# Kernel optimization log

Hardware: AMD Instinct MI355X
Metric: run time of the kernel (lower is better)

## Reference

```python
import jax, jax.numpy as jnp
import numpy as np

D_K = 64  # hardcoded in source module

def setup_inputs() -> dict:
    key = jax.random.key(0)
    kq, kk, kv, km = jax.random.split(key, 4)
    B, H, S, D = 2, 16, 2048, D_K
    Q = jax.random.normal(kq, (B, H, S, D), dtype=jnp.float32)
    K = jax.random.normal(kk, (B, H, S, D), dtype=jnp.float32)
    V = jax.random.normal(kv, (B, H, S, D), dtype=jnp.float32)
    # boolean mask: True positions are masked out (filled with -1e9)
    attn_mask = jax.random.randint(km, (B, H, S, S), 0, 2) == 1
    return {"Q": Q, "K": K, "V": V, "attn_mask": attn_mask}

def reference(Q, K, V, attn_mask):
    scale = 1.0 / np.sqrt(D_K).astype(np.float32)
    # scores: [B, H, S, S]
    scores = jnp.einsum('bhqd,bhkd->bhqk', Q, K) * scale
    scores = jnp.where(attn_mask, jnp.float32(-1e9), scores)
    attn = jax.nn.softmax(scores, axis=-1)
    context = jnp.einsum('bhqk,bhkd->bhqd', attn, V)
    return context
```

## Files before the change

kernel.cpp:

```cpp
#include <hip/hip_runtime.h>

#define SEQ    2048
#define DK     64
#define QBLK   128
#define KVBLK  64
#define NTILE  (SEQ / KVBLK)
#define PITCH  72
#define PPITCH 72

typedef __attribute__((ext_vector_type(8))) __bf16 bf16x8;
typedef __attribute__((ext_vector_type(4))) __bf16 bf16x4;
typedef __attribute__((ext_vector_type(2))) __bf16 bf16x2;
typedef __attribute__((ext_vector_type(4))) float  f32x4;
typedef __attribute__((ext_vector_type(4))) int    i32x4;

template<int CTRL>
__device__ __forceinline__ float dpp_ror(float v) {
  int i = __builtin_bit_cast(int, v);
  int r = __builtin_amdgcn_update_dpp(i, i, CTRL, 0xf, 0xf, false);
  return __builtin_bit_cast(float, r);
}
__device__ __forceinline__ float grp16_max(float v) {
  v = fmaxf(v, dpp_ror<0x128>(v));
  v = fmaxf(v, dpp_ror<0x124>(v));
  v = fmaxf(v, dpp_ror<0x122>(v));
  v = fmaxf(v, dpp_ror<0x121>(v));
  return v;
}
__device__ __forceinline__ float grp16_sum(float v) {
  v += dpp_ror<0x128>(v);
  v += dpp_ror<0x124>(v);
  v += dpp_ror<0x122>(v);
  v += dpp_ror<0x121>(v);
  return v;
}

__device__ __forceinline__ void block_sync_lds() {
  asm volatile("s_waitcnt lgkmcnt(0)" ::: "memory");
  __builtin_amdgcn_sched_barrier(0);
  __builtin_amdgcn_s_barrier();
  __builtin_amdgcn_sched_barrier(0);
}

__global__ __launch_bounds__(256, 2)
void sdpa_fwd(const float* __restrict__ Q, const float* __restrict__ K,
              const float* __restrict__ V, const int* __restrict__ M,
              float* __restrict__ O)
{
  __shared__ __bf16 Klds[KVBLK][PITCH];
  __shared__ __bf16 Vt[DK][PITCH];
  __shared__ __bf16 Plds[4][32][PPITCH];

  const int tid  = threadIdx.x;
  const int w    = tid >> 6;
  const int lane = tid & 63;
  const int g    = lane >> 4;
  const int li   = lane & 15;

  const int bid = blockIdx.x;
  const int blk = (bid & 7) * 64 + (bid >> 3);
  const int qb  = blk & (SEQ / QBLK - 1);
  const int bh  = blk >> 4;

  const float* Qp = Q + (size_t)bh * SEQ * DK;
  const float* Kp = K + (size_t)bh * SEQ * DK;
  const float* Vp = V + (size_t)bh * SEQ * DK;
  const int*   Mp = M + (size_t)bh * SEQ * SEQ;
  float*       Op = O + (size_t)bh * SEQ * DK;

  const int q0 = qb * QBLK + w * 16;

  const int sk = tid >> 2;
  const int sd = (tid & 3) * 16;
  const int sj = ((sk & 3) << 4) | (sk >> 2);
  const int vk = (tid & 31) * 2;
  const int vd = (tid >> 5) * 8;

  bf16x8 qfrag[2][2];
  #pragma unroll
  for (int m = 0; m < 2; ++m) {
    const float qs = 0.125f * 1.44269504088896340736f;
    const float* qr = Qp + (size_t)(q0 + m * 64 + li) * DK + g * 8;
    #pragma unroll
    for (int h2 = 0; h2 < 2; ++h2) {
      f32x4 a = *(const f32x4*)(qr + h2 * 32);
      f32x4 b = *(const f32x4*)(qr + h2 * 32 + 4);
      bf16x8 f;
      #pragma unroll
      for (int e = 0; e < 4; ++e) { f[e] = (__bf16)(a[e] * qs); f[4 + e] = (__bf16)(b[e] * qs); }
      qfrag[m][h2] = f;
    }
  }

  f32x4 acc[2][4];
  #pragma unroll
  for (int m = 0; m < 2; ++m)
    #pragma unroll
    for (int c = 0; c < 4; ++c) acc[m][c] = (f32x4){0.f, 0.f, 0.f, 0.f};
  float m_r[2][4], l_r[2][4];
  #pragma unroll
  for (int m = 0; m < 2; ++m)
    #pragma unroll
    for (int r = 0; r < 4; ++r) { m_r[m][r] = -__builtin_inff(); l_r[m][r] = 0.f; }

  f32x4 kA[4], vA[4];
  i32x4 mA[8];

  {
    const float* ks  = Kp + (size_t)sk * DK + sd;
    const float* vs0 = Vp + (size_t)vk * DK + vd;
    const float* vs1 = Vp + (size_t)(vk + 1) * DK + vd;
    #pragma unroll
    for (int i = 0; i < 4; ++i) kA[i] = *(const f32x4*)(ks + 4 * i);
    vA[0] = *(const f32x4*)vs0; vA[1] = *(const f32x4*)(vs0 + 4);
    vA[2] = *(const f32x4*)vs1; vA[3] = *(const f32x4*)(vs1 + 4);
    #pragma unroll
    for (int m = 0; m < 2; ++m)
      #pragma unroll
      for (int r = 0; r < 4; ++r)
        mA[m * 4 + r] = __builtin_nontemporal_load(
            (const i32x4*)(Mp + (size_t)(q0 + m * 64 + 4 * g + r) * SEQ + li * 4));
  }

  for (int kt = 0; kt < NTILE; ++kt) {
    block_sync_lds();

    {
      bf16x8 klo, khi;
      #pragma unroll
      for (int e = 0; e < 4; ++e) {
        klo[e] = (__bf16)kA[0][e]; klo[4 + e] = (__bf16)kA[1][e];
        khi[e] = (__bf16)kA[2][e]; khi[4 + e] = (__bf16)kA[3][e];
      }
      *(bf16x8*)&Klds[sj][sd]     = klo;
      *(bf16x8*)&Klds[sj][sd + 8] = khi;
      #pragma unroll
      for (int j = 0; j < 4; ++j) {
        bf16x2 p0; p0[0] = (__bf16)vA[0][j]; p0[1] = (__bf16)vA[2][j];
        bf16x2 p1; p1[0] = (__bf16)vA[1][j]; p1[1] = (__bf16)vA[3][j];
        *(bf16x2*)&Vt[vd + j][vk]     = p0;
        *(bf16x2*)&Vt[vd + 4 + j][vk] = p1;
      }
    }

    const int tn = (kt + 1 < NTILE) ? kt + 1 : 0;

    {
      const float* ks  = Kp + (size_t)(tn * KVBLK + sk) * DK + sd;
      const float* vs0 = Vp + (size_t)(tn * KVBLK + vk) * DK + vd;
      const float* vs1 = Vp + (size_t)(tn * KVBLK + vk + 1) * DK + vd;
      #pragma unroll
      for (int i = 0; i < 4; ++i) kA[i] = *(const f32x4*)(ks + 4 * i);
      vA[0] = *(const f32x4*)vs0; vA[1] = *(const f32x4*)(vs0 + 4);
      vA[2] = *(const f32x4*)vs1; vA[3] = *(const f32x4*)(vs1 + 4);
    }

    block_sync_lds();

    #pragma unroll
    for (int m = 0; m < 2; ++m) {
      f32x4 st[4];
      #pragma unroll
      for (int nt = 0; nt < 4; ++nt) {
        bf16x8 b0 = *(const bf16x8*)&Klds[nt * 16 + li][g * 8];
        bf16x8 b1 = *(const bf16x8*)&Klds[nt * 16 + li][32 + g * 8];
        f32x4 s = (f32x4){0.f, 0.f, 0.f, 0.f};
        s = __builtin_amdgcn_mfma_f32_16x16x32_bf16(qfrag[m][0], b0, s, 0, 0, 0);
        s = __builtin_amdgcn_mfma_f32_16x16x32_bf16(qfrag[m][1], b1, s, 0, 0, 0);
        st[nt] = s;
      }

      #pragma unroll
      for (int r = 0; r < 4; ++r) {
        i32x4 mm = mA[m * 4 + r];
        mA[m * 4 + r] = __builtin_nontemporal_load(
            (const i32x4*)(Mp + (size_t)(q0 + m * 64 + 4 * g + r) * SEQ + tn * KVBLK + li * 4));
        float s0 = mm.x ? -1e9f : st[0][r];
        float s1 = mm.y ? -1e9f : st[1][r];
        float s2 = mm.z ? -1e9f : st[2][r];
        float s3 = mm.w ? -1e9f : st[3][r];
        float mx    = grp16_max(fmaxf(fmaxf(s0, s1), fmaxf(s2, s3)));
        float mnew  = fmaxf(m_r[m][r], mx);
        float alpha = __builtin_amdgcn_exp2f(m_r[m][r] - mnew);
        float p0 = __builtin_amdgcn_exp2f(s0 - mnew);
        float p1 = __builtin_amdgcn_exp2f(s1 - mnew);
        float p2 = __builtin_amdgcn_exp2f(s2 - mnew);
        float p3 = __builtin_amdgcn_exp2f(s3 - mnew);
        l_r[m][r] = l_r[m][r] * alpha + grp16_sum((p0 + p1) + (p2 + p3));
        m_r[m][r] = mnew;
        acc[m][0][r] *= alpha;
        acc[m][1][r] *= alpha;
        acc[m][2][r] *= alpha;
        acc[m][3][r] *= alpha;
        bf16x4 pk;
        pk[0] = (__bf16)p0; pk[1] = (__bf16)p1; pk[2] = (__bf16)p2; pk[3] = (__bf16)p3;
        *(bf16x4*)&Plds[w][m * 16 + 4 * g + r][li * 4] = pk;
      }
    }

    asm volatile("s_waitcnt lgkmcnt(0)" ::: "memory");
    __builtin_amdgcn_sched_barrier(0);

    #pragma unroll
    for (int dt = 0; dt < 4; ++dt) {
      bf16x8 v0 = *(const bf16x8*)&Vt[dt * 16 + li][g * 8];
      bf16x8 v1 = *(const bf16x8*)&Vt[dt * 16 + li][32 + g * 8];
      #pragma unroll
      for (int m = 0; m < 2; ++m) {
        bf16x8 pa0 = *(const bf16x8*)&Plds[w][m * 16 + li][g * 8];
        bf16x8 pa1 = *(const bf16x8*)&Plds[w][m * 16 + li][32 + g * 8];
        acc[m][dt] = __builtin_amdgcn_mfma_f32_16x16x32_bf16(pa0, v0, acc[m][dt], 0, 0, 0);
        acc[m][dt] = __builtin_amdgcn_mfma_f32_16x16x32_bf16(pa1, v1, acc[m][dt], 0, 0, 0);
      }
    }
  }

  #pragma unroll
  for (int m = 0; m < 2; ++m)
    #pragma unroll
    for (int r = 0; r < 4; ++r) {
      float inv = 1.0f / l_r[m][r];
      float* orow = Op + (size_t)(q0 + m * 64 + 4 * g + r) * DK + li;
      #pragma unroll
      for (int dt = 0; dt < 4; ++dt)
        __builtin_nontemporal_store(acc[m][dt][r] * inv, &orow[dt * 16]);
    }
}

extern "C" void kernel_launch(void* const* d_in, const int* in_sizes, int n_in,
                              void* d_out, int out_size, void* d_ws, size_t ws_size,
                              hipStream_t stream) {
  const float* Q = (const float*)d_in[0];
  const float* K = (const float*)d_in[1];
  const float* V = (const float*)d_in[2];
  const int*   M = (const int*)d_in[3];
  float*       O = (float*)d_out;

  const int nblocks = 2 * 16 * (SEQ / QBLK);
  sdpa_fwd<<<nblocks, 256, 0, stream>>>(Q, K, V, M, O);
}
```

Baseline: 725.0 us.

## Pre-pack boolean mask into bitmask before attention kernel

After: 845.8 us. 1.17x slower.

```diff
diff --git a/kernel.cpp b/kernel.cpp
--- a/kernel.cpp
+++ b/kernel.cpp
@@ -42,9 +42,29 @@
   __builtin_amdgcn_sched_barrier(0);
 }
 
+__global__ __launch_bounds__(256)
+void pack_mask(const int* __restrict__ M, unsigned short* __restrict__ W,
+               int nwords16) {
+  int idx    = blockIdx.x * 256 + threadIdx.x;
+  int stride = gridDim.x * 256;
+  for (int wi = idx; wi < nwords16; wi += stride) {
+    const i32x4* p = (const i32x4*)(M + (size_t)wi * 16);
+    unsigned bits = 0;
+    #pragma unroll
+    for (int j = 0; j < 4; ++j) {
+      i32x4 v = __builtin_nontemporal_load(p + j);
+      unsigned nib = (v.x != 0 ? 1u : 0u) | (v.y != 0 ? 2u : 0u) |
+                     (v.z != 0 ? 4u : 0u) | (v.w != 0 ? 8u : 0u);
+      bits |= nib << (j * 4);
+    }
+    __builtin_nontemporal_store((unsigned short)bits, &W[wi]);
+  }
+}
+
 __global__ __launch_bounds__(256, 2)
 void sdpa_fwd(const float* __restrict__ Q, const float* __restrict__ K,
-              const float* __restrict__ V, const int* __restrict__ M,
+              const float* __restrict__ V,
+              const unsigned long long* __restrict__ W,
               float* __restrict__ O)
 {
   __shared__ __bf16 Klds[KVBLK][PITCH];
@@ -56,6 +76,7 @@
   const int lane = tid & 63;
   const int g    = lane >> 4;
   const int li   = lane & 15;
+  const int li4  = li * 4;
 
   const int bid = blockIdx.x;
   const int blk = (bid & 7) * 64 + (bid >> 3);
@@ -65,7 +86,7 @@
   const float* Qp = Q + (size_t)bh * SEQ * DK;
   const float* Kp = K + (size_t)bh * SEQ * DK;
   const float* Vp = V + (size_t)bh * SEQ * DK;
-  const int*   Mp = M + (size_t)bh * SEQ * SEQ;
+  const unsigned long long* Wp = W + (size_t)bh * SEQ * (SEQ / 64);
   float*       Op = O + (size_t)bh * SEQ * DK;
 
   const int q0 = qb * QBLK + w * 16;
@@ -104,7 +125,7 @@
     for (int r = 0; r < 4; ++r) { m_r[m][r] = -__builtin_inff(); l_r[m][r] = 0.f; }
 
   f32x4 kA[4], vA[4];
-  i32x4 mA[8];
+  unsigned long long mw[8];
 
   {
     const float* ks  = Kp + (size_t)sk * DK + sd;
@@ -118,8 +139,7 @@
     for (int m = 0; m < 2; ++m)
       #pragma unroll
       for (int r = 0; r < 4; ++r)
-        mA[m * 4 + r] = __builtin_nontemporal_load(
-            (const i32x4*)(Mp + (size_t)(q0 + m * 64 + 4 * g + r) * SEQ + li * 4));
+        mw[m * 4 + r] = Wp[(size_t)(q0 + m * 64 + 4 * g + r) * (SEQ / 64)];
   }
 
   for (int kt = 0; kt < NTILE; ++kt) {
@@ -172,13 +192,12 @@
 
       #pragma unroll
       for (int r = 0; r < 4; ++r) {
-        i32x4 mm = mA[m * 4 + r];
-        mA[m * 4 + r] = __builtin_nontemporal_load(
-            (const i32x4*)(Mp + (size_t)(q0 + m * 64 + 4 * g + r) * SEQ + tn * KVBLK + li * 4));
-        float s0 = mm.x ? -1e9f : st[0][r];
-        float s1 = mm.y ? -1e9f : st[1][r];
-        float s2 = mm.z ? -1e9f : st[2][r];
-        float s3 = mm.w ? -1e9f : st[3][r];
+        const unsigned nib = (unsigned)(mw[m * 4 + r] >> li4) & 15u;
+        mw[m * 4 + r] = Wp[(size_t)(q0 + m * 64 + 4 * g + r) * (SEQ / 64) + tn];
+        float s0 = (nib & 1u) ? -1e9f : st[0][r];
+        float s1 = (nib & 2u) ? -1e9f : st[1][r];
+        float s2 = (nib & 4u) ? -1e9f : st[2][r];
+        float s3 = (nib & 8u) ? -1e9f : st[3][r];
         float mx    = grp16_max(fmaxf(fmaxf(s0, s1), fmaxf(s2, s3)));
         float mnew  = fmaxf(m_r[m][r], mx);
         float alpha = __builtin_amdgcn_exp2f(m_r[m][r] - mnew);
@@ -236,6 +255,10 @@
   const int*   M = (const int*)d_in[3];
   float*       O = (float*)d_out;
 
+  const int nwords16 = 2 * 16 * SEQ * (SEQ / 16);
+  pack_mask<<<2048, 256, 0, stream>>>(M, (unsigned short*)d_ws, nwords16);
+
   const int nblocks = 2 * 16 * (SEQ / QBLK);
-  sdpa_fwd<<<nblocks, 256, 0, stream>>>(Q, K, V, M, O);
-}
+  sdpa_fwd<<<nblocks, 256, 0, stream>>>(Q, K, V,
+                                        (const unsigned long long*)d_ws, O);
+}
```
